# Kernel tuning notes

Measured on AMD Instinct MI355X. Metric: run time of the kernel, lower is better.

## Reference

```python
import jax, jax.numpy as jnp
import numpy as np
from jax import lax

D = 33            # n_vertices
NEG_SLOPE = 0.2   # LeakyReLU slope
EPS_IN = 1e-5     # InstanceNorm eps


def _block(x, w, b, gamma, beta):
    # Conv2d(k=3, stride=2, pad=1) -> LeakyReLU(0.2) -> optional InstanceNorm2d(affine)
    y = lax.conv_general_dilated(x, w, (2, 2), [(1, 1), (1, 1)],
                                 dimension_numbers=('NCHW', 'OIHW', 'NCHW'))
    y = y + b[None, :, None, None]
    y = jnp.where(y >= 0, y, NEG_SLOPE * y)
    if gamma is not None:
        mu = jnp.mean(y, (2, 3), keepdims=True)
        var = jnp.var(y, (2, 3), keepdims=True)
        y = (y - mu) * lax.rsqrt(var + EPS_IN) * gamma[None, :, None, None] + beta[None, :, None, None]
    return y


def _backbone(lq, w1, b1, g1, be1, w2, b2, g2, be2, w3, b3, g3, be3,
              w4, b4, g4, be4, w5, b5):
    B = lq.shape[0]
    # F.interpolate(..., 256, bilinear, align_corners=False) == half-pixel linear, no antialias
    x = jax.image.resize(lq, (B, 3, 256, 256), method='linear', antialias=False)
    x = _block(x, w1, b1, g1, be1)   # [B,16,128,128]
    x = _block(x, w2, b2, g2, be2)   # [B,32,64,64]
    x = _block(x, w3, b3, g3, be3)   # [B,64,32,32]
    x = _block(x, w4, b4, g4, be4)   # [B,128,16,16]
    x = _block(x, w5, b5, None, None)  # [B,128,8,8]; Dropout is identity in eval
    # AdaptiveAvgPool2d(2) on 8x8 -> mean over 4x4 blocks
    x = x.reshape(B, 128, 2, 4, 2, 4).mean((3, 5))  # [B,128,2,2]
    return x.reshape(B, -1)  # [B,512]


def _trilerp(lut, r, g, b):
    # lut [3,D,D,D]; r,g,b [N] in [0, D-1]; align_corners=True + border padding
    i0 = jnp.clip(jnp.floor(r).astype(jnp.int32), 0, D - 2)
    j0 = jnp.clip(jnp.floor(g).astype(jnp.int32), 0, D - 2)
    k0 = jnp.clip(jnp.floor(b).astype(jnp.int32), 0, D - 2)
    fr, fg, fb = r - i0, g - j0, b - k0

    def c(di, dj, dk):
        return lut[:, i0 + di, j0 + dj, k0 + dk]  # [3,N]

    return (c(0, 0, 0) * (1 - fr) * (1 - fg) * (1 - fb)
            + c(0, 0, 1) * (1 - fr) * (1 - fg) * fb
            + c(0, 1, 0) * (1 - fr) * fg * (1 - fb)
            + c(0, 1, 1) * (1 - fr) * fg * fb
            + c(1, 0, 0) * fr * (1 - fg) * (1 - fb)
            + c(1, 0, 1) * fr * (1 - fg) * fb
            + c(1, 1, 0) * fr * fg * (1 - fb)
            + c(1, 1, 1) * fr * fg * fb)


def _ailut_transform(img, luts, vertices):
    # img [B,3,H,W] in [0,1]; luts [B,3,D,D,D]; vertices [B,3,D] sorted in [0,1]
    B, C, H, W = img.shape
    p = img.reshape(B, C, -1)  # [B,3,N]
    # per-(b,c) searchsorted(right=True)
    idx = jax.vmap(jax.vmap(lambda v, x: jnp.searchsorted(v, x, side='right')))(vertices, p)
    idx = jnp.clip(idx, 1, D - 1)
    v_lo = jnp.take_along_axis(vertices, idx - 1, axis=-1)
    v_hi = jnp.take_along_axis(vertices, idx, axis=-1)
    frac = (p - v_lo) / (v_hi - v_lo + 1e-8)
    coord = (idx - 1).astype(img.dtype) + frac        # [B,3,N] in [0, D-1]
    coord = jnp.clip(coord, 0.0, D - 1.0)             # border padding
    # torch grid layout (blue->W, green->H, red->D); LUT axes are (red, green, blue)
    sampled = jax.vmap(_trilerp)(luts, coord[:, 0], coord[:, 1], coord[:, 2])  # [B,3,N]
    return sampled.reshape(B, C, H, W)


def _forward(lq, w1, b1, g1, be1, w2, b2, g2, be2, w3, b3, g3, be3,
             w4, b4, g4, be4, w5, b5, lw, lb, bw, aw, ab):
    B = lq.shape[0]
    codes = _backbone(lq, w1, b1, g1, be1, w2, b2, g2, be2, w3, b3, g3, be3,
                      w4, b4, g4, be4, w5, b5)          # [B,512]
    # LUTGenerator
    weights = codes @ lw.T + lb                          # [B,3]
    luts = (weights @ bw.T).reshape(B, 3, D, D, D)       # [B,3,D,D,D]
    # AdaInt
    intervals = (codes @ aw.T + ab).reshape(B, 3, D - 1)
    intervals = jax.nn.softmax(intervals, axis=-1)
    vertices = jnp.pad(jnp.cumsum(intervals, axis=-1), ((0, 0), (0, 0), (1, 0)))  # [B,3,D]
    outs = jnp.clip(_ailut_transform(lq, luts, vertices), 0.0, 1.0)
    return outs, weights, vertices


def setup_inputs() -> dict:
    key = jax.random.key(0)
    ks = jax.random.split(key, 16)
    B = 4
    lq = jax.random.uniform(ks[0], (B, 3, 1024, 1024), jnp.float32)

    def cw(k, o, i):
        return jax.random.normal(k, (o, i, 3, 3), jnp.float32) * (1.0 / np.sqrt(i * 9))

    w1 = cw(ks[1], 16, 3);   b1 = jnp.zeros(16);  g1 = jnp.ones(16);  be1 = jnp.zeros(16)
    w2 = cw(ks[2], 32, 16);  b2 = jnp.zeros(32);  g2 = jnp.ones(32);  be2 = jnp.zeros(32)
    w3 = cw(ks[3], 64, 32);  b3 = jnp.zeros(64);  g3 = jnp.ones(64);  be3 = jnp.zeros(64)
    w4 = cw(ks[4], 128, 64); b4 = jnp.zeros(128); g4 = jnp.ones(128); be4 = jnp.zeros(128)
    w5 = cw(ks[5], 128, 128); b5 = jnp.zeros(128)

    lw = jax.random.normal(ks[6], (3, 512), jnp.float32) * 0.02
    lb = jnp.ones(3, jnp.float32)  # init: bias = ones
    # basis LUT bank: rank0 = identity LUT (meshgrid/(D-1), channel-flipped), others small
    grid = jnp.stack(jnp.meshgrid(jnp.arange(D), jnp.arange(D), jnp.arange(D),
                                  indexing='ij'), 0).astype(jnp.float32) / (D - 1)
    identity = grid[::-1].reshape(-1, 1)  # [3*D^3,1]
    bw = jnp.concatenate([identity,
                          jax.random.normal(ks[7], (3 * D ** 3, 2), jnp.float32) * 0.01], axis=1)
    aw = jax.random.normal(ks[8], (96, 512), jnp.float32) * 0.01
    ab = jnp.ones(96, jnp.float32)  # init: bias = ones
    return {'lq': lq, 'w1': w1, 'b1': b1, 'g1': g1, 'be1': be1,
            'w2': w2, 'b2': b2, 'g2': g2, 'be2': be2,
            'w3': w3, 'b3': b3, 'g3': g3, 'be3': be3,
            'w4': w4, 'b4': b4, 'g4': g4, 'be4': be4,
            'w5': w5, 'b5': b5, 'lw': lw, 'lb': lb, 'bw': bw, 'aw': aw, 'ab': ab}


def reference(lq, w1, b1, g1, be1, w2, b2, g2, be2, w3, b3, g3, be3,
              w4, b4, g4, be4, w5, b5, lw, lb, bw, aw, ab):
    return _forward(lq, w1, b1, g1, be1, w2, b2, g2, be2, w3, b3, g3, be3,
                    w4, b4, g4, be4, w5, b5, lw, lb, bw, aw, ab)
```

## Files before the change

### kernel.cpp

```cpp
#include <hip/hip_runtime.h>
#include <hip/hip_fp16.h>
#include <math.h>

#define LUT_D 33
#define LUT_D3 35937
#define NEG 0.2f
#define BATCH 4
#define HW_IMG 1048576

__global__ void k_resize(const float* __restrict__ lq, float* __restrict__ out) {
    int gid = blockIdx.x * 256 + threadIdx.x;
    if (gid >= BATCH * 3 * 256 * 64) return;
    int xq = gid & 63;
    int y  = (gid >> 6) & 255;
    int pc = gid >> 14;
    const float* ra = lq + (size_t)pc * HW_IMG + (size_t)(4 * y + 1) * 1024 + xq * 16;
    const float4* pa = (const float4*)ra;
    const float4* pb = (const float4*)(ra + 1024);
    float4 a0 = pa[0], a1 = pa[1], a2 = pa[2], a3 = pa[3];
    float4 b0 = pb[0], b1 = pb[1], b2 = pb[2], b3 = pb[3];
    float4 o;
    o.x = 0.25f * (a0.y + a0.z + b0.y + b0.z);
    o.y = 0.25f * (a1.y + a1.z + b1.y + b1.z);
    o.z = 0.25f * (a2.y + a2.z + b2.y + b2.z);
    o.w = 0.25f * (a3.y + a3.z + b3.y + b3.z);
    ((float4*)out)[gid] = o;
}

template<int IC, int OC, int OH, int OW, int NSPLIT, bool NORM_IN, bool STATS_OUT>
__global__ void __launch_bounds__(256) k_conv_t(
    const float* __restrict__ in, const float* __restrict__ nrm_in,
    const float* __restrict__ w, const float* __restrict__ bias,
    float* __restrict__ out, float* __restrict__ part) {
    constexpr int IH = OH * 2, IW = OW * 2;
    constexpr int ICB = IC / NSPLIT;
    constexpr int TROW = 20, TSZ = 17 * TROW;
    constexpr int WQ = ICB * 9 / 4;
    constexpr int NTX = OW / 8, NTY = OH / 8, NOCG = OC / 16;
    constexpr int NT = NTX * NTY;
    constexpr int PX = OH * OW;

    __shared__ float sIn[ICB * TSZ];
    __shared__ float swl[16 * ICB * 9];
    __shared__ float sNm[NORM_IN ? ICB * 2 : 1];

    int id = blockIdx.x;
    int ocg   = id % NOCG;   id /= NOCG;
    int icc_i = id % NSPLIT; id /= NSPLIT;
    int tx    = id % NTX;    id /= NTX;
    int ty    = id % NTY;    id /= NTY;
    int b     = id;
    int icc   = icc_i * ICB;

    int t    = threadIdx.x;
    int lane = t >> 6;
    int px   = t & 63;
    int py   = px >> 3, pxx = px & 7;
    int oc0  = ocg * 16 + lane * 4;

    if (IC == ICB) {
        const float4* wsrc = (const float4*)(w + (size_t)ocg * 16 * IC * 9);
        for (int i = t; i < 16 * IC * 9 / 4; i += 256) ((float4*)swl)[i] = wsrc[i];
    } else {
        for (int i = t; i < 16 * WQ; i += 256) {
            int ol = i / WQ, qi = i % WQ;
            ((float4*)swl)[ol * WQ + qi] =
                *(const float4*)(w + ((size_t)(ocg * 16 + ol) * IC + icc) * 9 + qi * 4);
        }
    }
    if (NORM_IN) {
        for (int i = t; i < ICB * 2; i += 256) sNm[i] = nrm_in[(b * IC + icc) * 2 + i];
    }
    __syncthreads();

    int iy0 = ty * 16 - 1;
    int xbase = tx * 16;
    const float* inb = in + (size_t)(b * IC + icc) * (IH * IW);
    for (int q = t; q < ICB * 17 * 4; q += 256) {
        int ic_l = q / 68;
        int r    = q % 68;
        int row  = r >> 2, quad = r & 3;
        int iy = iy0 + row;
        float4 v = {0.f, 0.f, 0.f, 0.f};
        if (iy >= 0 && iy < IH) {
            v = *(const float4*)(inb + (size_t)ic_l * (IH * IW) + (size_t)iy * IW + xbase + quad * 4);
            if (NORM_IN) {
                float sc = sNm[ic_l * 2], sh = sNm[ic_l * 2 + 1];
                v.x = v.x * sc + sh; v.y = v.y * sc + sh;
                v.z = v.z * sc + sh; v.w = v.w * sc + sh;
            }
        }
        *(float4*)(sIn + ic_l * TSZ + row * TROW + 4 + quad * 4) = v;
    }
    for (int h = t; h < ICB * 17; h += 256) {
        int ic_l = h / 17, row = h % 17;
        int iy = iy0 + row, ix = xbase - 1;
        float v = 0.f;
        if (iy >= 0 && iy < IH && ix >= 0) {
            v = inb[(size_t)ic_l * (IH * IW) + (size_t)iy * IW + ix];
            if (NORM_IN) v = v * sNm[ic_l * 2] + sNm[ic_l * 2 + 1];
        }
        sIn[ic_l * TSZ + row * TROW + 3] = v;
    }
    __syncthreads();

    float acc[4];
    #pragma unroll
    for (int j = 0; j < 4; j++) acc[j] = (NSPLIT == 1) ? bias[oc0 + j] : 0.f;

    for (int i2 = 0; i2 < ICB; i2++) {
        const float* tp = sIn + i2 * TSZ + py * 2 * TROW + pxx * 2 + 3;
        float x0 = tp[0],        x1 = tp[1],        x2 = tp[2];
        float x3 = tp[TROW],     x4 = tp[TROW + 1], x5 = tp[TROW + 2];
        float x6 = tp[2 * TROW], x7 = tp[2 * TROW + 1], x8 = tp[2 * TROW + 2];
        #pragma unroll
        for (int j = 0; j < 4; j++) {
            const float* wp = swl + ((lane * 4 + j) * ICB + i2) * 9;
            acc[j] = fmaf(x0, wp[0], acc[j]);
            acc[j] = fmaf(x1, wp[1], acc[j]);
            acc[j] = fmaf(x2, wp[2], acc[j]);
            acc[j] = fmaf(x3, wp[3], acc[j]);
            acc[j] = fmaf(x4, wp[4], acc[j]);
            acc[j] = fmaf(x5, wp[5], acc[j]);
            acc[j] = fmaf(x6, wp[6], acc[j]);
            acc[j] = fmaf(x7, wp[7], acc[j]);
            acc[j] = fmaf(x8, wp[8], acc[j]);
        }
    }

    int oy = ty * 8 + py, ox = tx * 8 + pxx;
    if (NSPLIT == 1) {
        int tile = ty * NTX + tx;
        #pragma unroll
        for (int j = 0; j < 4; j++) {
            float a = acc[j];
            a = a >= 0.f ? a : NEG * a;
            out[((size_t)(b * OC + oc0 + j) * OH + oy) * OW + ox] = a;
            if (STATS_OUT) {
                float s1 = a, s2 = a * a;
                for (int off = 32; off > 0; off >>= 1) {
                    s1 += __shfl_down(s1, off, 64);
                    s2 += __shfl_down(s2, off, 64);
                }
                if (px == 0) {
                    size_t pi = ((size_t)(b * OC + oc0 + j) * NT + tile) * 2;
                    part[pi] = s1; part[pi + 1] = s2;
                }
            }
        }
    } else {
        #pragma unroll
        for (int j = 0; j < 4; j++) {
            part[(size_t)icc_i * (BATCH * OC * PX) +
                 (size_t)(b * OC + oc0 + j) * PX + oy * OW + ox] = acc[j];
        }
    }
}

template<int NSPLIT, int OC, int PX, bool STATS>
__global__ void k_combine(const float* __restrict__ ps, const float* __restrict__ bias,
                          float* __restrict__ out, float* __restrict__ spart) {
    constexpr int TOT = BATCH * OC * PX;
    int e = blockIdx.x * 256 + threadIdx.x;
    if (e >= TOT) return;
    float s = 0.f;
    #pragma unroll
    for (int k = 0; k < NSPLIT; k++) s += ps[(size_t)k * TOT + e];
    int oc = (e / PX) % OC;
    s += bias[oc];
    s = s >= 0.f ? s : NEG * s;
    out[e] = s;
    if (STATS) {
        float s1 = s, s2 = s * s;
        for (int off = 32; off > 0; off >>= 1) {
            s1 += __shfl_down(s1, off, 64);
            s2 += __shfl_down(s2, off, 64);
        }
        if ((threadIdx.x & 63) == 0) {
            int widx = e >> 6;
            spart[widx * 2] = s1; spart[widx * 2 + 1] = s2;
        }
    }
}

template<int NT>
__global__ void k_norm(const float* __restrict__ part, const float* __restrict__ g,
                       const float* __restrict__ be, float invN, int C,
                       float* __restrict__ nrm) {
    int bc = blockIdx.x;
    int t  = threadIdx.x;
    float s1 = 0.f, s2 = 0.f;
    for (int i = t; i < NT; i += 64) {
        s1 += part[((size_t)bc * NT + i) * 2];
        s2 += part[((size_t)bc * NT + i) * 2 + 1];
    }
    #pragma unroll
    for (int off = 32; off > 0; off >>= 1) {
        s1 += __shfl_down(s1, off, 64);
        s2 += __shfl_down(s2, off, 64);
    }
    if (t == 0) {
        int c = bc % C;
        float m   = s1 * invN;
        float var = s2 * invN - m * m;
        float sc  = g[c] * rsqrtf(var + 1e-5f);
        nrm[bc * 2]     = sc;
        nrm[bc * 2 + 1] = be[c] - m * sc;
    }
}

__global__ void k_pool(const float* __restrict__ f5, float* __restrict__ codes) {
    int c = blockIdx.x * 256 + threadIdx.x;
    if (c >= 2048) return;
    int b = c >> 9;
    int rest = c & 511;
    int oc = rest >> 2, q = rest & 3;
    int py = (q >> 1) * 4, px = (q & 1) * 4;
    const float* p = f5 + ((size_t)(b * 128 + oc)) * 64;
    float s = 0.f;
    #pragma unroll
    for (int dy = 0; dy < 4; dy++)
        #pragma unroll
        for (int dx = 0; dx < 4; dx++)
            s += p[(py + dy) * 8 + px + dx];
    codes[c] = s * (1.f / 16.f);
}

__global__ void k_head(const float* __restrict__ codes, const float* __restrict__ lw,
                       const float* __restrict__ lb, const float* __restrict__ aw,
                       const float* __restrict__ ab, float* __restrict__ wt,
                       float* __restrict__ vert, float* __restrict__ tabA,
                       float* __restrict__ tabC, float* __restrict__ out_w,
                       float* __restrict__ out_v) {
    int blk = blockIdx.x;
    int t = threadIdx.x;
    if (blk == 12) {
        if (t < 48) {
            int j = t >> 2, q = t & 3;
            int b = j / 3, jj = j % 3;
            const float4* c4 = (const float4*)(codes + b * 512 + q * 128);
            const float4* l4 = (const float4*)(lw + jj * 512 + q * 128);
            float s = 0.f;
            for (int k = 0; k < 32; k++) {
                float4 cv = c4[k], lv = l4[k];
                s += cv.x * lv.x + cv.y * lv.y + cv.z * lv.z + cv.w * lv.w;
            }
            s += __shfl_down(s, 2, 64);
            s += __shfl_down(s, 1, 64);
            if (q == 0) {
                s += lb[jj];
                wt[j] = s;
                out_w[j] = s;
            }
        }
        return;
    }
    int b = blk / 3, ch = blk % 3;
    __shared__ float y[32];
    __shared__ float vsh[33];
    {
        int m = t & 31, half = t >> 5;
        const float4* c4 = (const float4*)(codes + b * 512 + half * 256);
        const float4* a4 = (const float4*)(aw + (size_t)(ch * 32 + m) * 512 + half * 256);
        float s = (half == 0) ? ab[ch * 32 + m] : 0.f;
        for (int k = 0; k < 64; k++) {
            float4 cv = c4[k], av = a4[k];
            s += cv.x * av.x + cv.y * av.y + cv.z * av.z + cv.w * av.w;
        }
        s += __shfl_down(s, 32, 64);
        if (half == 0) y[m] = s;
    }
    __syncthreads();
    if (t == 0) {
        float mx = y[0];
        for (int m = 1; m < 32; m++) mx = fmaxf(mx, y[m]);
        float e[32];
        float sum = 0.f;
        for (int m = 0; m < 32; m++) { e[m] = expf(y[m] - mx); sum += e[m]; }
        float inv = 1.f / sum;
        float cum = 0.f;
        float* vb = vert + (b * 3 + ch) * 33;
        float* ob = out_v + (b * 3 + ch) * 33;
        vb[0] = 0.f; ob[0] = 0.f; vsh[0] = 0.f;
        for (int m = 0; m < 32; m++) {
            cum += e[m] * inv;
            vb[m + 1] = cum; ob[m + 1] = cum; vsh[m + 1] = cum;
        }
    }
    __syncthreads();
    float4* A4 = ((float4*)tabA) + (b * 3 + ch) * 256;
    float*  C1 = tabC + (b * 3 + ch) * 256;
    for (int u = t; u < 256; u += 64) {
        float lo = (float)u * (1.f / 256.f);
        float hi = (float)(u + 1) * (1.f / 256.f);
        int n0 = 0, nin = 0;
        float vs = 2.0f;
        #pragma unroll
        for (int m = 0; m < 33; m++) {
            float vm = vsh[m];
            n0 += (vm <= lo) ? 1 : 0;
            if (vm > lo && vm < hi) { if (nin == 0) vs = vm; nin++; }
        }
        int i0 = n0 < 1 ? 1 : (n0 > 32 ? 32 : n0);
        int i1 = (n0 + 1) < 1 ? 1 : ((n0 + 1) > 32 ? 32 : (n0 + 1));
        float m0 = 1.f / (vsh[i0] - vsh[i0 - 1] + 1e-8f);
        float c0 = (float)(i0 - 1) - vsh[i0 - 1] * m0;
        float m1 = 1.f / (vsh[i1] - vsh[i1 - 1] + 1e-8f);
        float c1 = (float)(i1 - 1) - vsh[i1 - 1] * m1;
        if (nin >= 2) { vs = 2.0f; m0 = __int_as_float(0x7fc00000); c0 = 0.f; }
        A4[u] = make_float4(vs, m0, c0, m1);
        C1[u] = c1;
    }
}

__global__ void k_lutgen(const float* __restrict__ bw, const float* __restrict__ wt,
                         float4* __restrict__ lutp) {
    int gid = blockIdx.x * 256 + threadIdx.x;
    if (gid >= BATCH * LUT_D3) return;
    int b = gid / LUT_D3;
    int cell = gid - b * LUT_D3;
    int k = cell % LUT_D;
    int cn = (k < LUT_D - 1) ? cell + 1 : cell;
    float w0 = wt[b * 3], w1 = wt[b * 3 + 1], w2 = wt[b * 3 + 2];
    const float* r0p = bw + (size_t)(0 * LUT_D3 + cell) * 3;
    const float* g0p = bw + (size_t)(1 * LUT_D3 + cell) * 3;
    const float* b0p = bw + (size_t)(2 * LUT_D3 + cell) * 3;
    const float* r1p = bw + (size_t)(0 * LUT_D3 + cn) * 3;
    const float* g1p = bw + (size_t)(1 * LUT_D3 + cn) * 3;
    const float* b1p = bw + (size_t)(2 * LUT_D3 + cn) * 3;
    union { float4 f4; __half h[8]; } u;
    u.h[0] = __float2half_rn(r0p[0] * w0 + r0p[1] * w1 + r0p[2] * w2);
    u.h[1] = __float2half_rn(g0p[0] * w0 + g0p[1] * w1 + g0p[2] * w2);
    u.h[2] = __float2half_rn(b0p[0] * w0 + b0p[1] * w1 + b0p[2] * w2);
    u.h[3] = __float2half_rn(r1p[0] * w0 + r1p[1] * w1 + r1p[2] * w2);
    u.h[4] = __float2half_rn(g1p[0] * w0 + g1p[1] * w1 + g1p[2] * w2);
    u.h[5] = __float2half_rn(b1p[0] * w0 + b1p[1] * w1 + b1p[2] * w2);
    u.h[6] = __float2half_rn(0.f);
    u.h[7] = __float2half_rn(0.f);
    lutp[gid] = u.f4;
}

__global__ void k_cellgen(const float4* __restrict__ lutp, float4* __restrict__ cells) {
    int gid = blockIdx.x * 256 + threadIdx.x;
    if (gid >= BATCH * 32768) return;
    int b = gid >> 15;
    int cell = gid & 32767;
    int k0 = cell & 31, j0 = (cell >> 5) & 31, i0 = cell >> 10;
    const float4* L = lutp + (size_t)b * LUT_D3;
    int base = (i0 * LUT_D + j0) * LUT_D + k0;
    float4 e00 = L[base];
    float4 e01 = L[base + LUT_D];
    float4 e10 = L[base + LUT_D * LUT_D];
    float4 e11 = L[base + LUT_D * LUT_D + LUT_D];
    float4 o0, o1, o2;
    o0.x = e00.x; o0.y = e00.y; o0.z = e00.z;
    o0.w = e01.x; o1.x = e01.y; o1.y = e01.z;
    o1.z = e10.x; o1.w = e10.y; o2.x = e10.z;
    o2.y = e11.x; o2.z = e11.y; o2.w = e11.z;
    float4* dst = cells + (size_t)gid * 4;
    dst[0] = o0; dst[1] = o1; dst[2] = o2;
}

__device__ __forceinline__ void searchL(const float4* __restrict__ A,
                                        const float* __restrict__ C,
                                        const float* __restrict__ v33,
                                        float x, int& i0, float& f) {
    int u = (int)(x * 256.f);
    u = u < 0 ? 0 : (u > 255 ? 255 : u);
    float4 e = A[u];
    float c1 = C[u];
    float coord = (x < e.x) ? fmaf(e.y, x, e.z) : fmaf(e.w, x, c1);
    if (!(coord == coord)) {
        int lo = 0, hi = LUT_D;
        while (lo < hi) { int mid = (lo + hi) >> 1; if (v33[mid] <= x) lo = mid + 1; else hi = mid; }
        int idx = lo < 1 ? 1 : (lo > LUT_D - 1 ? LUT_D - 1 : lo);
        float vl = v33[idx - 1], vh = v33[idx];
        coord = (float)(idx - 1) + (x - vl) / (vh - vl + 1e-8f);
    }
    coord = fminf(fmaxf(coord, 0.f), (float)(LUT_D - 1));
    i0 = (int)coord;
    if (i0 > LUT_D - 2) i0 = LUT_D - 2;
    f = coord - (float)i0;
}

__device__ __forceinline__ void decode_lerp3(float wa, float wb, float wc, float fb,
                                             float& rv, float& gv, float& bv) {
    union { float f; __half2 h; } u0, u1, u2;
    u0.f = wa; u1.f = wb; u2.f = wc;
    float2 a = __half22float2(u0.h);
    float2 b = __half22float2(u1.h);
    float2 c = __half22float2(u2.h);
    rv = fmaf(fb, b.y - a.x, a.x);
    gv = fmaf(fb, c.x - a.y, a.y);
    bv = fmaf(fb, c.y - b.x, b.x);
}

__global__ void __launch_bounds__(256) k_transform(const float* __restrict__ lq,
                                                   const float4* __restrict__ cells,
                                                   const float* __restrict__ vert,
                                                   const float* __restrict__ gA,
                                                   const float* __restrict__ gC,
                                                   float* __restrict__ out) {
    int bimg = blockIdx.x >> 10;
    int blk  = blockIdx.x & 1023;
    __shared__ float4 sA[3 * 256];
    __shared__ float  sC[3 * 256];
    __shared__ float  sv[3 * LUT_D + 1];

    int p0 = blk * 1024 + threadIdx.x * 4;
    const float* lr = lq + (size_t)bimg * 3 * HW_IMG + p0;
    float4 r4 = *(const float4*)(lr);
    float4 g4 = *(const float4*)(lr + HW_IMG);
    float4 b4 = *(const float4*)(lr + 2 * HW_IMG);

    const float4* gA4 = (const float4*)gA;
    for (int i = threadIdx.x; i < 768; i += 256) sA[i] = gA4[bimg * 768 + i];
    for (int i = threadIdx.x; i < 192; i += 256)
        ((float4*)sC)[i] = ((const float4*)gC)[bimg * 192 + i];
    if (threadIdx.x < 99) sv[threadIdx.x] = vert[bimg * 99 + threadIdx.x];
    __syncthreads();

    float rr[4] = {r4.x, r4.y, r4.z, r4.w};
    float gg[4] = {g4.x, g4.y, g4.z, g4.w};
    float bb[4] = {b4.x, b4.y, b4.z, b4.w};

    int cidx[4];
    float fra[4], fga[4], fba[4];
    #pragma unroll
    for (int i = 0; i < 4; i++) {
        int i0, j0, k0;
        searchL(sA,       sC,       sv,      rr[i], i0, fra[i]);
        searchL(sA + 256, sC + 256, sv + 33, gg[i], j0, fga[i]);
        searchL(sA + 512, sC + 512, sv + 66, bb[i], k0, fba[i]);
        cidx[i] = ((i0 * 32 + j0) << 5) + k0;
    }
    float4 c0[4], c1[4], c2[4];
    #pragma unroll
    for (int i = 0; i < 4; i++) {
        const float4* p = cells + (((size_t)(bimg << 15) + cidx[i]) << 2);
        c0[i] = p[0]; c1[i] = p[1]; c2[i] = p[2];
    }
    float ro[4], go[4], bo[4];
    #pragma unroll
    for (int i = 0; i < 4; i++) {
        float fb = fba[i];
        float r00, g00, b00, r01, g01, b01, r10, g10, b10, r11, g11, b11;
        decode_lerp3(c0[i].x, c0[i].y, c0[i].z, fb, r00, g00, b00);
        decode_lerp3(c0[i].w, c1[i].x, c1[i].y, fb, r01, g01, b01);
        decode_lerp3(c1[i].z, c1[i].w, c2[i].x, fb, r10, g10, b10);
        decode_lerp3(c2[i].y, c2[i].z, c2[i].w, fb, r11, g11, b11);
        float fr = fra[i], fg = fga[i];
        float w00 = (1.f - fr) * (1.f - fg), w01 = (1.f - fr) * fg;
        float w10 = fr * (1.f - fg),         w11 = fr * fg;
        float rx = r00 * w00 + r01 * w01 + r10 * w10 + r11 * w11;
        float ry = g00 * w00 + g01 * w01 + g10 * w10 + g11 * w11;
        float rz = b00 * w00 + b01 * w01 + b10 * w10 + b11 * w11;
        ro[i] = fminf(fmaxf(rx, 0.f), 1.f);
        go[i] = fminf(fmaxf(ry, 0.f), 1.f);
        bo[i] = fminf(fmaxf(rz, 0.f), 1.f);
    }
    float* op = out + (size_t)bimg * 3 * HW_IMG + p0;
    float4 o0 = {ro[0], ro[1], ro[2], ro[3]};
    float4 o1 = {go[0], go[1], go[2], go[3]};
    float4 o2 = {bo[0], bo[1], bo[2], bo[3]};
    *(float4*)(op) = o0;
    *(float4*)(op + HW_IMG) = o1;
    *(float4*)(op + 2 * HW_IMG) = o2;
}

extern "C" void kernel_launch(void* const* d_in, const int* in_sizes, int n_in,
                              void* d_out, int out_size, void* d_ws, size_t ws_size,
                              hipStream_t stream) {
    const float* lq  = (const float*)d_in[0];
    const float* w1  = (const float*)d_in[1];
    const float* b1  = (const float*)d_in[2];
    const float* g1  = (const float*)d_in[3];
    const float* be1 = (const float*)d_in[4];
    const float* w2  = (const float*)d_in[5];
    const float* b2  = (const float*)d_in[6];
    const float* g2  = (const float*)d_in[7];
    const float* be2 = (const float*)d_in[8];
    const float* w3  = (const float*)d_in[9];
    const float* b3  = (const float*)d_in[10];
    const float* g3  = (const float*)d_in[11];
    const float* be3 = (const float*)d_in[12];
    const float* w4  = (const float*)d_in[13];
    const float* b4  = (const float*)d_in[14];
    const float* g4  = (const float*)d_in[15];
    const float* be4 = (const float*)d_in[16];
    const float* w5  = (const float*)d_in[17];
    const float* b5  = (const float*)d_in[18];
    const float* lw  = (const float*)d_in[19];
    const float* lb  = (const float*)d_in[20];
    const float* bw  = (const float*)d_in[21];
    const float* aw  = (const float*)d_in[22];
    const float* ab  = (const float*)d_in[23];

    float* ws     = (float*)d_ws;
    float* r256   = ws;
    float* f1     = r256 + 786432;
    float* f2     = f1 + 1048576;
    float* f3     = f2 + 524288;
    float* f4     = f3 + 262144;
    float* f5     = f4 + 131072;
    float* codes  = f5 + 32768;
    float* wt     = codes + 2048;
    float* vert   = wt + 12;
    float* part1  = vert + 396;
    float* part2  = part1 + 32768;
    float* part3  = part2 + 16384;
    float* spart4 = part3 + 8192;
    float* norm1  = spart4 + 4096;
    float* norm2  = norm1 + 128;
    float* norm3  = norm2 + 256;
    float* norm4  = norm3 + 512;
    float* tabA   = norm4 + 1024;
    float* tabC   = tabA + 12288;
    float* luts4  = tabC + 3072;
    float* psplit4 = f1;
    float* psplit5 = f1 + 524288;
    float* cells  = ws;

    float* outs  = (float*)d_out;
    float* out_w = outs + (size_t)BATCH * 3 * HW_IMG;
    float* out_v = out_w + 12;

    k_resize<<<768, 256, 0, stream>>>(lq, r256);
    k_conv_t<3, 16, 128, 128, 1, false, true><<<1024, 256, 0, stream>>>(
        r256, nullptr, w1, b1, f1, part1);
    k_norm<256><<<64, 64, 0, stream>>>(part1, g1, be1, 1.f / 16384.f, 16, norm1);
    k_conv_t<16, 32, 64, 64, 1, true, true><<<512, 256, 0, stream>>>(
        f1, norm1, w2, b2, f2, part2);
    k_norm<64><<<128, 64, 0, stream>>>(part2, g2, be2, 1.f / 4096.f, 32, norm2);
    k_conv_t<32, 64, 32, 32, 1, true, true><<<256, 256, 0, stream>>>(
        f2, norm2, w3, b3, f3, part3);
    k_norm<16><<<256, 64, 0, stream>>>(part3, g3, be3, 1.f / 1024.f, 64, norm3);
    k_conv_t<64, 128, 16, 16, 4, true, false><<<512, 256, 0, stream>>>(
        f3, norm3, w4, b4, nullptr, psplit4);
    k_combine<4, 128, 256, true><<<512, 256, 0, stream>>>(psplit4, b4, f4, spart4);
    k_norm<4><<<512, 64, 0, stream>>>(spart4, g4, be4, 1.f / 256.f, 128, norm4);
    k_conv_t<128, 128, 8, 8, 8, true, false><<<256, 256, 0, stream>>>(
        f4, norm4, w5, b5, nullptr, psplit5);
    k_combine<8, 128, 64, false><<<128, 256, 0, stream>>>(psplit5, b5, f5, nullptr);
    k_pool<<<8, 256, 0, stream>>>(f5, codes);
    k_head<<<13, 64, 0, stream>>>(codes, lw, lb, aw, ab, wt, vert, tabA, tabC, out_w, out_v);
    k_lutgen<<<(BATCH * LUT_D3 + 255) / 256, 256, 0, stream>>>(bw, wt, (float4*)luts4);
    k_cellgen<<<512, 256, 0, stream>>>((const float4*)luts4, (float4*)cells);
    k_transform<<<BATCH * 1024, 256, 0, stream>>>(
        lq, (const float4*)cells, vert, tabA, tabC, outs);
}
```

Before: 284.3 us.

## Fuse resize, norm, split-combine, pool and LUT generation into fewer kernels

Folds the resize into the first conv's tile load, computes the instance-norm scale and shift inside each consumer conv from the partial sums, and replaces the input-channel split plus combine kernels with in-block channel chunking. Pooling moves into the head kernel, LUT generation and cell packing merge into one kernel that emits half-precision cells, and the search tables are repacked into a single five-float layout. The transform kernel also remaps block indices by XCD. Launch count drops from 17 to 8, but the late conv layers now run with only 128 and 32 blocks, which leaves much of the GPU idle, and fp16 cells lose LUT precision.

Measured after the change: 326.8 us. +15.0%, slower.

```diff
diff --git a/kernel.cpp b/kernel.cpp
--- a/kernel.cpp
+++ b/kernel.cpp
@@ -8,49 +8,27 @@
 #define BATCH 4
 #define HW_IMG 1048576
 
-__global__ void k_resize(const float* __restrict__ lq, float* __restrict__ out) {
-    int gid = blockIdx.x * 256 + threadIdx.x;
-    if (gid >= BATCH * 3 * 256 * 64) return;
-    int xq = gid & 63;
-    int y  = (gid >> 6) & 255;
-    int pc = gid >> 14;
-    const float* ra = lq + (size_t)pc * HW_IMG + (size_t)(4 * y + 1) * 1024 + xq * 16;
-    const float4* pa = (const float4*)ra;
-    const float4* pb = (const float4*)(ra + 1024);
-    float4 a0 = pa[0], a1 = pa[1], a2 = pa[2], a3 = pa[3];
-    float4 b0 = pb[0], b1 = pb[1], b2 = pb[2], b3 = pb[3];
-    float4 o;
-    o.x = 0.25f * (a0.y + a0.z + b0.y + b0.z);
-    o.y = 0.25f * (a1.y + a1.z + b1.y + b1.z);
-    o.z = 0.25f * (a2.y + a2.z + b2.y + b2.z);
-    o.w = 0.25f * (a3.y + a3.z + b3.y + b3.z);
-    ((float4*)out)[gid] = o;
-}
-
-template<int IC, int OC, int OH, int OW, int NSPLIT, bool NORM_IN, bool STATS_OUT>
-__global__ void __launch_bounds__(256) k_conv_t(
-    const float* __restrict__ in, const float* __restrict__ nrm_in,
+template<int IC, int OC, int OH, int OW, int ICCH, bool NORM_IN, bool RESIZE_IN, bool STATS_OUT>
+__global__ void __launch_bounds__(256) k_conv2(
+    const float* __restrict__ in, const float* __restrict__ part_in,
+    const float* __restrict__ g, const float* __restrict__ be, float invN, int ntin,
     const float* __restrict__ w, const float* __restrict__ bias,
-    float* __restrict__ out, float* __restrict__ part) {
+    float* __restrict__ out, float* __restrict__ part_out) {
     constexpr int IH = OH * 2, IW = OW * 2;
-    constexpr int ICB = IC / NSPLIT;
+    constexpr int NCH = IC / ICCH;
     constexpr int TROW = 20, TSZ = 17 * TROW;
-    constexpr int WQ = ICB * 9 / 4;
     constexpr int NTX = OW / 8, NTY = OH / 8, NOCG = OC / 16;
     constexpr int NT = NTX * NTY;
-    constexpr int PX = OH * OW;
-
-    __shared__ float sIn[ICB * TSZ];
-    __shared__ float swl[16 * ICB * 9];
-    __shared__ float sNm[NORM_IN ? ICB * 2 : 1];
+
+    __shared__ float sIn[ICCH * TSZ];
+    __shared__ float swl[16 * ICCH * 9];
+    __shared__ float sNm[NORM_IN ? IC * 2 : 1];
 
     int id = blockIdx.x;
-    int ocg   = id % NOCG;   id /= NOCG;
-    int icc_i = id % NSPLIT; id /= NSPLIT;
-    int tx    = id % NTX;    id /= NTX;
-    int ty    = id % NTY;    id /= NTY;
-    int b     = id;
-    int icc   = icc_i * ICB;
+    int ocg = id % NOCG;  id /= NOCG;
+    int tx  = id % NTX;   id /= NTX;
+    int ty  = id % NTY;   id /= NTY;
+    int b   = id;
 
     int t    = threadIdx.x;
     int lane = t >> 6;
@@ -58,187 +36,187 @@
     int py   = px >> 3, pxx = px & 7;
     int oc0  = ocg * 16 + lane * 4;
 
-    if (IC == ICB) {
-        const float4* wsrc = (const float4*)(w + (size_t)ocg * 16 * IC * 9);
-        for (int i = t; i < 16 * IC * 9 / 4; i += 256) ((float4*)swl)[i] = wsrc[i];
-    } else {
-        for (int i = t; i < 16 * WQ; i += 256) {
-            int ol = i / WQ, qi = i % WQ;
-            ((float4*)swl)[ol * WQ + qi] =
-                *(const float4*)(w + ((size_t)(ocg * 16 + ol) * IC + icc) * 9 + qi * 4);
-        }
-    }
     if (NORM_IN) {
-        for (int i = t; i < ICB * 2; i += 256) sNm[i] = nrm_in[(b * IC + icc) * 2 + i];
-    }
-    __syncthreads();
+        constexpr int P = 256 / IC;
+        int c = t / P, r = t % P;
+        float s1 = 0.f, s2 = 0.f;
+        for (int i = r; i < ntin; i += P) {
+            const float* pp = part_in + ((size_t)(b * IC + c) * ntin + i) * 2;
+            s1 += pp[0]; s2 += pp[1];
+        }
+        #pragma unroll
+        for (int off = P >> 1; off > 0; off >>= 1) {
+            s1 += __shfl_down(s1, off, 64);
+            s2 += __shfl_down(s2, off, 64);
+        }
+        if (r == 0) {
+            float m   = s1 * invN;
+            float var = s2 * invN - m * m;
+            float sc  = g[c] * rsqrtf(var + 1e-5f);
+            sNm[c * 2]     = sc;
+            sNm[c * 2 + 1] = be[c] - m * sc;
+        }
+        __syncthreads();
+    }
+
+    float acc[4];
+    #pragma unroll
+    for (int j = 0; j < 4; j++) acc[j] = bias[oc0 + j];
 
     int iy0 = ty * 16 - 1;
     int xbase = tx * 16;
-    const float* inb = in + (size_t)(b * IC + icc) * (IH * IW);
-    for (int q = t; q < ICB * 17 * 4; q += 256) {
-        int ic_l = q / 68;
-        int r    = q % 68;
-        int row  = r >> 2, quad = r & 3;
-        int iy = iy0 + row;
-        float4 v = {0.f, 0.f, 0.f, 0.f};
-        if (iy >= 0 && iy < IH) {
-            v = *(const float4*)(inb + (size_t)ic_l * (IH * IW) + (size_t)iy * IW + xbase + quad * 4);
-            if (NORM_IN) {
-                float sc = sNm[ic_l * 2], sh = sNm[ic_l * 2 + 1];
-                v.x = v.x * sc + sh; v.y = v.y * sc + sh;
-                v.z = v.z * sc + sh; v.w = v.w * sc + sh;
-            }
-        }
-        *(float4*)(sIn + ic_l * TSZ + row * TROW + 4 + quad * 4) = v;
-    }
-    for (int h = t; h < ICB * 17; h += 256) {
-        int ic_l = h / 17, row = h % 17;
-        int iy = iy0 + row, ix = xbase - 1;
-        float v = 0.f;
-        if (iy >= 0 && iy < IH && ix >= 0) {
-            v = inb[(size_t)ic_l * (IH * IW) + (size_t)iy * IW + ix];
-            if (NORM_IN) v = v * sNm[ic_l * 2] + sNm[ic_l * 2 + 1];
-        }
-        sIn[ic_l * TSZ + row * TROW + 3] = v;
-    }
-    __syncthreads();
-
-    float acc[4];
-    #pragma unroll
-    for (int j = 0; j < 4; j++) acc[j] = (NSPLIT == 1) ? bias[oc0 + j] : 0.f;
-
-    for (int i2 = 0; i2 < ICB; i2++) {
-        const float* tp = sIn + i2 * TSZ + py * 2 * TROW + pxx * 2 + 3;
-        float x0 = tp[0],        x1 = tp[1],        x2 = tp[2];
-        float x3 = tp[TROW],     x4 = tp[TROW + 1], x5 = tp[TROW + 2];
-        float x6 = tp[2 * TROW], x7 = tp[2 * TROW + 1], x8 = tp[2 * TROW + 2];
-        #pragma unroll
-        for (int j = 0; j < 4; j++) {
-            const float* wp = swl + ((lane * 4 + j) * ICB + i2) * 9;
-            acc[j] = fmaf(x0, wp[0], acc[j]);
-            acc[j] = fmaf(x1, wp[1], acc[j]);
-            acc[j] = fmaf(x2, wp[2], acc[j]);
-            acc[j] = fmaf(x3, wp[3], acc[j]);
-            acc[j] = fmaf(x4, wp[4], acc[j]);
-            acc[j] = fmaf(x5, wp[5], acc[j]);
-            acc[j] = fmaf(x6, wp[6], acc[j]);
-            acc[j] = fmaf(x7, wp[7], acc[j]);
-            acc[j] = fmaf(x8, wp[8], acc[j]);
+
+    for (int ch = 0; ch < NCH; ch++) {
+        int icc = ch * ICCH;
+        if (ch) __syncthreads();
+
+        if (IC == ICCH) {
+            const float4* wsrc = (const float4*)(w + (size_t)ocg * 16 * IC * 9);
+            for (int i = t; i < 16 * IC * 9 / 4; i += 256) ((float4*)swl)[i] = wsrc[i];
+        } else {
+            constexpr int WQ = ICCH * 9 / 4;
+            for (int i = t; i < 16 * WQ; i += 256) {
+                int ol = i / WQ, qi = i % WQ;
+                ((float4*)swl)[ol * WQ + qi] =
+                    *(const float4*)(w + ((size_t)(ocg * 16 + ol) * IC + icc) * 9 + qi * 4);
+            }
+        }
+
+        if (RESIZE_IN) {
+            for (int q = t; q < ICCH * 17 * 4; q += 256) {
+                int ic_l = q / 68;
+                int r2   = q % 68;
+                int row  = r2 >> 2, quad = r2 & 3;
+                int iy = iy0 + row;
+                float4 v = {0.f, 0.f, 0.f, 0.f};
+                if (iy >= 0 && iy < IH) {
+                    const float* lb_ = in + (size_t)(b * IC + icc + ic_l) * HW_IMG
+                                          + (size_t)(4 * iy + 1) * 1024;
+                    int c0 = (xbase + quad * 4) * 4;
+                    const float4* pa = (const float4*)(lb_ + c0);
+                    const float4* pb = (const float4*)(lb_ + 1024 + c0);
+                    float4 a0 = pa[0], a1 = pa[1], a2 = pa[2], a3 = pa[3];
+                    float4 q0 = pb[0], q1 = pb[1], q2 = pb[2], q3 = pb[3];
+                    v.x = 0.25f * (a0.y + a0.z + q0.y + q0.z);
+                    v.y = 0.25f * (a1.y + a1.z + q1.y + q1.z);
+                    v.z = 0.25f * (a2.y + a2.z + q2.y + q2.z);
+                    v.w = 0.25f * (a3.y + a3.z + q3.y + q3.z);
+                }
+                *(float4*)(sIn + ic_l * TSZ + row * TROW + 4 + quad * 4) = v;
+            }
+            for (int h = t; h < ICCH * 17; h += 256) {
+                int ic_l = h / 17, row = h % 17;
+                int iy = iy0 + row, ix = xbase - 1;
+                float v = 0.f;
+                if (iy >= 0 && iy < IH && ix >= 0) {
+                    const float* lb_ = in + (size_t)(b * IC + icc + ic_l) * HW_IMG
+                                          + (size_t)(4 * iy + 1) * 1024;
+                    float4 a = *(const float4*)(lb_ + ix * 4);
+                    float4 q0 = *(const float4*)(lb_ + 1024 + ix * 4);
+                    v = 0.25f * (a.y + a.z + q0.y + q0.z);
+                }
+                sIn[ic_l * TSZ + row * TROW + 3] = v;
+            }
+        } else {
+            const float* inb = in + (size_t)(b * IC + icc) * (IH * IW);
+            for (int q = t; q < ICCH * 17 * 4; q += 256) {
+                int ic_l = q / 68;
+                int r2   = q % 68;
+                int row  = r2 >> 2, quad = r2 & 3;
+                int iy = iy0 + row;
+                float4 v = {0.f, 0.f, 0.f, 0.f};
+                if (iy >= 0 && iy < IH) {
+                    v = *(const float4*)(inb + (size_t)ic_l * (IH * IW)
+                                             + (size_t)iy * IW + xbase + quad * 4);
+                    if (NORM_IN) {
+                        float sc = sNm[(icc + ic_l) * 2], sh = sNm[(icc + ic_l) * 2 + 1];
+                        v.x = v.x * sc + sh; v.y = v.y * sc + sh;
+                        v.z = v.z * sc + sh; v.w = v.w * sc + sh;
+                    }
+                }
+                *(float4*)(sIn + ic_l * TSZ + row * TROW + 4 + quad * 4) = v;
+            }
+            for (int h = t; h < ICCH * 17; h += 256) {
+                int ic_l = h / 17, row = h % 17;
+                int iy = iy0 + row, ix = xbase - 1;
+                float v = 0.f;
+                if (iy >= 0 && iy < IH && ix >= 0) {
+                    v = inb[(size_t)ic_l * (IH * IW) + (size_t)iy * IW + ix];
+                    if (NORM_IN) v = v * sNm[(icc + ic_l) * 2] + sNm[(icc + ic_l) * 2 + 1];
+                }
+                sIn[ic_l * TSZ + row * TROW + 3] = v;
+            }
+        }
+        __syncthreads();
+
+        for (int i2 = 0; i2 < ICCH; i2++) {
+            const float* tp = sIn + i2 * TSZ + py * 2 * TROW + pxx * 2 + 3;
+            float x0 = tp[0],        x1 = tp[1],        x2 = tp[2];
+            float x3 = tp[TROW],     x4 = tp[TROW + 1], x5 = tp[TROW + 2];
+            float x6 = tp[2 * TROW], x7 = tp[2 * TROW + 1], x8 = tp[2 * TROW + 2];
+            #pragma unroll
+            for (int j = 0; j < 4; j++) {
+                const float* wp = swl + ((lane * 4 + j) * ICCH + i2) * 9;
+                acc[j] = fmaf(x0, wp[0], acc[j]);
+                acc[j] = fmaf(x1, wp[1], acc[j]);
+                acc[j] = fmaf(x2, wp[2], acc[j]);
+                acc[j] = fmaf(x3, wp[3], acc[j]);
+                acc[j] = fmaf(x4, wp[4], acc[j]);
+                acc[j] = fmaf(x5, wp[5], acc[j]);
+                acc[j] = fmaf(x6, wp[6], acc[j]);
+                acc[j] = fmaf(x7, wp[7], acc[j]);
+                acc[j] = fmaf(x8, wp[8], acc[j]);
+            }
         }
     }
 
     int oy = ty * 8 + py, ox = tx * 8 + pxx;
-    if (NSPLIT == 1) {
-        int tile = ty * NTX + tx;
-        #pragma unroll
-        for (int j = 0; j < 4; j++) {
-            float a = acc[j];
-            a = a >= 0.f ? a : NEG * a;
-            out[((size_t)(b * OC + oc0 + j) * OH + oy) * OW + ox] = a;
-            if (STATS_OUT) {
-                float s1 = a, s2 = a * a;
-                for (int off = 32; off > 0; off >>= 1) {
-                    s1 += __shfl_down(s1, off, 64);
-                    s2 += __shfl_down(s2, off, 64);
-                }
-                if (px == 0) {
-                    size_t pi = ((size_t)(b * OC + oc0 + j) * NT + tile) * 2;
-                    part[pi] = s1; part[pi + 1] = s2;
-                }
-            }
-        }
-    } else {
-        #pragma unroll
-        for (int j = 0; j < 4; j++) {
-            part[(size_t)icc_i * (BATCH * OC * PX) +
-                 (size_t)(b * OC + oc0 + j) * PX + oy * OW + ox] = acc[j];
-        }
-    }
-}
-
-template<int NSPLIT, int OC, int PX, bool STATS>
-__global__ void k_combine(const float* __restrict__ ps, const float* __restrict__ bias,
-                          float* __restrict__ out, float* __restrict__ spart) {
-    constexpr int TOT = BATCH * OC * PX;
-    int e = blockIdx.x * 256 + threadIdx.x;
-    if (e >= TOT) return;
-    float s = 0.f;
-    #pragma unroll
-    for (int k = 0; k < NSPLIT; k++) s += ps[(size_t)k * TOT + e];
-    int oc = (e / PX) % OC;
-    s += bias[oc];
-    s = s >= 0.f ? s : NEG * s;
-    out[e] = s;
-    if (STATS) {
-        float s1 = s, s2 = s * s;
-        for (int off = 32; off > 0; off >>= 1) {
-            s1 += __shfl_down(s1, off, 64);
-            s2 += __shfl_down(s2, off, 64);
-        }
-        if ((threadIdx.x & 63) == 0) {
-            int widx = e >> 6;
-            spart[widx * 2] = s1; spart[widx * 2 + 1] = s2;
-        }
-    }
-}
-
-template<int NT>
-__global__ void k_norm(const float* __restrict__ part, const float* __restrict__ g,
-                       const float* __restrict__ be, float invN, int C,
-                       float* __restrict__ nrm) {
-    int bc = blockIdx.x;
-    int t  = threadIdx.x;
-    float s1 = 0.f, s2 = 0.f;
-    for (int i = t; i < NT; i += 64) {
-        s1 += part[((size_t)bc * NT + i) * 2];
-        s2 += part[((size_t)bc * NT + i) * 2 + 1];
-    }
-    #pragma unroll
-    for (int off = 32; off > 0; off >>= 1) {
-        s1 += __shfl_down(s1, off, 64);
-        s2 += __shfl_down(s2, off, 64);
-    }
-    if (t == 0) {
-        int c = bc % C;
-        float m   = s1 * invN;
-        float var = s2 * invN - m * m;
-        float sc  = g[c] * rsqrtf(var + 1e-5f);
-        nrm[bc * 2]     = sc;
-        nrm[bc * 2 + 1] = be[c] - m * sc;
-    }
-}
-
-__global__ void k_pool(const float* __restrict__ f5, float* __restrict__ codes) {
-    int c = blockIdx.x * 256 + threadIdx.x;
-    if (c >= 2048) return;
-    int b = c >> 9;
-    int rest = c & 511;
-    int oc = rest >> 2, q = rest & 3;
-    int py = (q >> 1) * 4, px = (q & 1) * 4;
-    const float* p = f5 + ((size_t)(b * 128 + oc)) * 64;
-    float s = 0.f;
-    #pragma unroll
-    for (int dy = 0; dy < 4; dy++)
-        #pragma unroll
-        for (int dx = 0; dx < 4; dx++)
-            s += p[(py + dy) * 8 + px + dx];
-    codes[c] = s * (1.f / 16.f);
-}
-
-__global__ void k_head(const float* __restrict__ codes, const float* __restrict__ lw,
+    int tile = ty * NTX + tx;
+    #pragma unroll
+    for (int j = 0; j < 4; j++) {
+        float a = acc[j];
+        a = a >= 0.f ? a : NEG * a;
+        out[((size_t)(b * OC + oc0 + j) * OH + oy) * OW + ox] = a;
+        if (STATS_OUT) {
+            float s1 = a, s2 = a * a;
+            for (int off = 32; off > 0; off >>= 1) {
+                s1 += __shfl_down(s1, off, 64);
+                s2 += __shfl_down(s2, off, 64);
+            }
+            if (px == 0) {
+                size_t pi = ((size_t)(b * OC + oc0 + j) * NT + tile) * 2;
+                part_out[pi] = s1; part_out[pi + 1] = s2;
+            }
+        }
+    }
+}
+
+__global__ void k_head(const float* __restrict__ f5, const float* __restrict__ lw,
                        const float* __restrict__ lb, const float* __restrict__ aw,
                        const float* __restrict__ ab, float* __restrict__ wt,
-                       float* __restrict__ vert, float* __restrict__ tabA,
-                       float* __restrict__ tabC, float* __restrict__ out_w,
-                       float* __restrict__ out_v) {
+                       float* __restrict__ vert, float* __restrict__ gT,
+                       float* __restrict__ out_w, float* __restrict__ out_v) {
     int blk = blockIdx.x;
     int t = threadIdx.x;
     if (blk == 12) {
+        __shared__ float sc2[2048];
+        for (int s = t; s < 2048; s += 64) {
+            int b = s >> 9, rest = s & 511, oc = rest >> 2, q = rest & 3;
+            int py = (q >> 1) * 4, pxq = (q & 1) * 4;
+            const float* p = f5 + (size_t)(b * 128 + oc) * 64;
+            float sum = 0.f;
+            #pragma unroll
+            for (int dy = 0; dy < 4; dy++) {
+                float4 v = *(const float4*)(p + (py + dy) * 8 + pxq);
+                sum += v.x + v.y + v.z + v.w;
+            }
+            sc2[s] = sum * (1.f / 16.f);
+        }
+        __syncthreads();
         if (t < 48) {
             int j = t >> 2, q = t & 3;
             int b = j / 3, jj = j % 3;
-            const float4* c4 = (const float4*)(codes + b * 512 + q * 128);
+            const float4* c4 = (const float4*)(sc2 + b * 512 + q * 128);
             const float4* l4 = (const float4*)(lw + jj * 512 + q * 128);
             float s = 0.f;
             for (int k = 0; k < 32; k++) {
@@ -247,20 +225,30 @@
             }
             s += __shfl_down(s, 2, 64);
             s += __shfl_down(s, 1, 64);
-            if (q == 0) {
-                s += lb[jj];
-                wt[j] = s;
-                out_w[j] = s;
-            }
+            if (q == 0) { s += lb[jj]; wt[j] = s; out_w[j] = s; }
         }
         return;
     }
     int b = blk / 3, ch = blk % 3;
+    __shared__ float scode[512];
     __shared__ float y[32];
     __shared__ float vsh[33];
+    for (int s = t; s < 512; s += 64) {
+        int oc = s >> 2, q = s & 3;
+        int py = (q >> 1) * 4, pxq = (q & 1) * 4;
+        const float* p = f5 + (size_t)(b * 128 + oc) * 64;
+        float sum = 0.f;
+        #pragma unroll
+        for (int dy = 0; dy < 4; dy++) {
+            float4 v = *(const float4*)(p + (py + dy) * 8 + pxq);
+            sum += v.x + v.y + v.z + v.w;
+        }
+        scode[s] = sum * (1.f / 16.f);
+    }
+    __syncthreads();
     {
         int m = t & 31, half = t >> 5;
-        const float4* c4 = (const float4*)(codes + b * 512 + half * 256);
+        const float4* c4 = (const float4*)(scode + half * 256);
         const float4* a4 = (const float4*)(aw + (size_t)(ch * 32 + m) * 512 + half * 256);
         float s = (half == 0) ? ab[ch * 32 + m] : 0.f;
         for (int k = 0; k < 64; k++) {
@@ -288,8 +276,7 @@
         }
     }
     __syncthreads();
-    float4* A4 = ((float4*)tabA) + (b * 3 + ch) * 256;
-    float*  C1 = tabC + (b * 3 + ch) * 256;
+    float* T = gT + (size_t)(b * 3 + ch) * 1280;
     for (int u = t; u < 256; u += 64) {
         float lo = (float)u * (1.f / 256.f);
         float hi = (float)(u + 1) * (1.f / 256.f);
@@ -308,68 +295,54 @@
         float m1 = 1.f / (vsh[i1] - vsh[i1 - 1] + 1e-8f);
         float c1 = (float)(i1 - 1) - vsh[i1 - 1] * m1;
         if (nin >= 2) { vs = 2.0f; m0 = __int_as_float(0x7fc00000); c0 = 0.f; }
-        A4[u] = make_float4(vs, m0, c0, m1);
-        C1[u] = c1;
-    }
-}
-
-__global__ void k_lutgen(const float* __restrict__ bw, const float* __restrict__ wt,
-                         float4* __restrict__ lutp) {
-    int gid = blockIdx.x * 256 + threadIdx.x;
-    if (gid >= BATCH * LUT_D3) return;
-    int b = gid / LUT_D3;
-    int cell = gid - b * LUT_D3;
-    int k = cell % LUT_D;
-    int cn = (k < LUT_D - 1) ? cell + 1 : cell;
-    float w0 = wt[b * 3], w1 = wt[b * 3 + 1], w2 = wt[b * 3 + 2];
-    const float* r0p = bw + (size_t)(0 * LUT_D3 + cell) * 3;
-    const float* g0p = bw + (size_t)(1 * LUT_D3 + cell) * 3;
-    const float* b0p = bw + (size_t)(2 * LUT_D3 + cell) * 3;
-    const float* r1p = bw + (size_t)(0 * LUT_D3 + cn) * 3;
-    const float* g1p = bw + (size_t)(1 * LUT_D3 + cn) * 3;
-    const float* b1p = bw + (size_t)(2 * LUT_D3 + cn) * 3;
-    union { float4 f4; __half h[8]; } u;
-    u.h[0] = __float2half_rn(r0p[0] * w0 + r0p[1] * w1 + r0p[2] * w2);
-    u.h[1] = __float2half_rn(g0p[0] * w0 + g0p[1] * w1 + g0p[2] * w2);
-    u.h[2] = __float2half_rn(b0p[0] * w0 + b0p[1] * w1 + b0p[2] * w2);
-    u.h[3] = __float2half_rn(r1p[0] * w0 + r1p[1] * w1 + r1p[2] * w2);
-    u.h[4] = __float2half_rn(g1p[0] * w0 + g1p[1] * w1 + g1p[2] * w2);
-    u.h[5] = __float2half_rn(b1p[0] * w0 + b1p[1] * w1 + b1p[2] * w2);
-    u.h[6] = __float2half_rn(0.f);
-    u.h[7] = __float2half_rn(0.f);
-    lutp[gid] = u.f4;
-}
-
-__global__ void k_cellgen(const float4* __restrict__ lutp, float4* __restrict__ cells) {
+        T[u * 5]     = vs;
+        T[u * 5 + 1] = m0;
+        T[u * 5 + 2] = c0;
+        T[u * 5 + 3] = m1;
+        T[u * 5 + 4] = c1;
+    }
+}
+
+__global__ void k_cells(const float* __restrict__ bw, const float* __restrict__ wtp,
+                        float4* __restrict__ cells) {
     int gid = blockIdx.x * 256 + threadIdx.x;
     if (gid >= BATCH * 32768) return;
     int b = gid >> 15;
     int cell = gid & 32767;
     int k0 = cell & 31, j0 = (cell >> 5) & 31, i0 = cell >> 10;
-    const float4* L = lutp + (size_t)b * LUT_D3;
-    int base = (i0 * LUT_D + j0) * LUT_D + k0;
-    float4 e00 = L[base];
-    float4 e01 = L[base + LUT_D];
-    float4 e10 = L[base + LUT_D * LUT_D];
-    float4 e11 = L[base + LUT_D * LUT_D + LUT_D];
-    float4 o0, o1, o2;
-    o0.x = e00.x; o0.y = e00.y; o0.z = e00.z;
-    o0.w = e01.x; o1.x = e01.y; o1.y = e01.z;
-    o1.z = e10.x; o1.w = e10.y; o2.x = e10.z;
-    o2.y = e11.x; o2.z = e11.y; o2.w = e11.z;
+    float w0 = wtp[b * 3], w1 = wtp[b * 3 + 1], w2 = wtp[b * 3 + 2];
+    int ci[4] = { (i0 * 33 + j0) * 33 + k0,
+                  (i0 * 33 + j0 + 1) * 33 + k0,
+                  ((i0 + 1) * 33 + j0) * 33 + k0,
+                  ((i0 + 1) * 33 + j0 + 1) * 33 + k0 };
+    float h[24];
+    #pragma unroll
+    for (int c = 0; c < 4; c++) {
+        #pragma unroll
+        for (int kk = 0; kk < 2; kk++) {
+            int id2 = ci[c] + kk;
+            #pragma unroll
+            for (int pl = 0; pl < 3; pl++) {
+                const float* p = bw + ((size_t)(pl * LUT_D3 + id2)) * 3;
+                h[c * 6 + kk * 3 + pl] = p[0] * w0 + p[1] * w1 + p[2] * w2;
+            }
+        }
+    }
+    union { float4 f4[3]; __half hh[24]; } u;
+    #pragma unroll
+    for (int i = 0; i < 24; i++) u.hh[i] = __float2half_rn(h[i]);
     float4* dst = cells + (size_t)gid * 4;
-    dst[0] = o0; dst[1] = o1; dst[2] = o2;
-}
-
-__device__ __forceinline__ void searchL(const float4* __restrict__ A,
-                                        const float* __restrict__ C,
-                                        const float* __restrict__ v33,
-                                        float x, int& i0, float& f) {
+    dst[0] = u.f4[0]; dst[1] = u.f4[1]; dst[2] = u.f4[2];
+}
+
+__device__ __forceinline__ void searchL5(const float* __restrict__ T,
+                                         const float* __restrict__ v33,
+                                         float x, int& i0, float& f) {
     int u = (int)(x * 256.f);
     u = u < 0 ? 0 : (u > 255 ? 255 : u);
-    float4 e = A[u];
-    float c1 = C[u];
-    float coord = (x < e.x) ? fmaf(e.y, x, e.z) : fmaf(e.w, x, c1);
+    const float* e = T + u * 5;
+    float vs = e[0];
+    float coord = (x < vs) ? fmaf(e[1], x, e[2]) : fmaf(e[3], x, e[4]);
     if (!(coord == coord)) {
         int lo = 0, hi = LUT_D;
         while (lo < hi) { int mid = (lo + hi) >> 1; if (v33[mid] <= x) lo = mid + 1; else hi = mid; }
@@ -398,14 +371,15 @@
 __global__ void __launch_bounds__(256) k_transform(const float* __restrict__ lq,
                                                    const float4* __restrict__ cells,
                                                    const float* __restrict__ vert,
-                                                   const float* __restrict__ gA,
-                                                   const float* __restrict__ gC,
+                                                   const float* __restrict__ gT,
                                                    float* __restrict__ out) {
-    int bimg = blockIdx.x >> 10;
-    int blk  = blockIdx.x & 1023;
-    __shared__ float4 sA[3 * 256];
-    __shared__ float  sC[3 * 256];
-    __shared__ float  sv[3 * LUT_D + 1];
+    int orig = blockIdx.x;
+    int xcd  = orig & 7;
+    int bimg = xcd >> 1;
+    int blk  = ((orig >> 3) << 1) | (xcd & 1);
+
+    __shared__ float sT[3840];
+    __shared__ float sv[100];
 
     int p0 = blk * 1024 + threadIdx.x * 4;
     const float* lr = lq + (size_t)bimg * 3 * HW_IMG + p0;
@@ -413,10 +387,7 @@
     float4 g4 = *(const float4*)(lr + HW_IMG);
     float4 b4 = *(const float4*)(lr + 2 * HW_IMG);
 
-    const float4* gA4 = (const float4*)gA;
-    for (int i = threadIdx.x; i < 768; i += 256) sA[i] = gA4[bimg * 768 + i];
-    for (int i = threadIdx.x; i < 192; i += 256)
-        ((float4*)sC)[i] = ((const float4*)gC)[bimg * 192 + i];
+    for (int i = threadIdx.x; i < 3840; i += 256) sT[i] = gT[bimg * 3840 + i];
     if (threadIdx.x < 99) sv[threadIdx.x] = vert[bimg * 99 + threadIdx.x];
     __syncthreads();
 
@@ -429,9 +400,9 @@
     #pragma unroll
     for (int i = 0; i < 4; i++) {
         int i0, j0, k0;
-        searchL(sA,       sC,       sv,      rr[i], i0, fra[i]);
-        searchL(sA + 256, sC + 256, sv + 33, gg[i], j0, fga[i]);
-        searchL(sA + 512, sC + 512, sv + 66, bb[i], k0, fba[i]);
+        searchL5(sT,        sv,      rr[i], i0, fra[i]);
+        searchL5(sT + 1280, sv + 33, gg[i], j0, fga[i]);
+        searchL5(sT + 2560, sv + 66, bb[i], k0, fba[i]);
         cidx[i] = ((i0 * 32 + j0) << 5) + k0;
     }
     float4 c0[4], c1[4], c2[4];
@@ -496,56 +467,37 @@
     const float* aw  = (const float*)d_in[22];
     const float* ab  = (const float*)d_in[23];
 
-    float* ws     = (float*)d_ws;
-    float* r256   = ws;
-    float* f1     = r256 + 786432;
-    float* f2     = f1 + 1048576;
-    float* f3     = f2 + 524288;
-    float* f4     = f3 + 262144;
-    float* f5     = f4 + 131072;
-    float* codes  = f5 + 32768;
-    float* wt     = codes + 2048;
-    float* vert   = wt + 12;
-    float* part1  = vert + 396;
-    float* part2  = part1 + 32768;
-    float* part3  = part2 + 16384;
-    float* spart4 = part3 + 8192;
-    float* norm1  = spart4 + 4096;
-    float* norm2  = norm1 + 128;
-    float* norm3  = norm2 + 256;
-    float* norm4  = norm3 + 512;
-    float* tabA   = norm4 + 1024;
-    float* tabC   = tabA + 12288;
-    float* luts4  = tabC + 3072;
-    float* psplit4 = f1;
-    float* psplit5 = f1 + 524288;
-    float* cells  = ws;
+    float* ws    = (float*)d_ws;
+    float* cells = ws;
+    float* f1    = ws;
+    float* f2    = f1 + 1048576;
+    float* f3    = f2 + 524288;
+    float* f4    = f3 + 262144;
+    float* f5    = f4 + 131072;
+    float* tail  = ws + 2097152;
+    float* wt    = tail;
+    float* vert  = wt + 12;
+    float* part1 = vert + 396;
+    float* part2 = part1 + 32768;
+    float* part3 = part2 + 16384;
+    float* part4 = part3 + 8192;
+    float* gT    = part4 + 4096;
 
     float* outs  = (float*)d_out;
     float* out_w = outs + (size_t)BATCH * 3 * HW_IMG;
     float* out_v = out_w + 12;
 
-    k_resize<<<768, 256, 0, stream>>>(lq, r256);
-    k_conv_t<3, 16, 128, 128, 1, false, true><<<1024, 256, 0, stream>>>(
-        r256, nullptr, w1, b1, f1, part1);
-    k_norm<256><<<64, 64, 0, stream>>>(part1, g1, be1, 1.f / 16384.f, 16, norm1);
-    k_conv_t<16, 32, 64, 64, 1, true, true><<<512, 256, 0, stream>>>(
-        f1, norm1, w2, b2, f2, part2);
-    k_norm<64><<<128, 64, 0, stream>>>(part2, g2, be2, 1.f / 4096.f, 32, norm2);
-    k_conv_t<32, 64, 32, 32, 1, true, true><<<256, 256, 0, stream>>>(
-        f2, norm2, w3, b3, f3, part3);
-    k_norm<16><<<256, 64, 0, stream>>>(part3, g3, be3, 1.f / 1024.f, 64, norm3);
-    k_conv_t<64, 128, 16, 16, 4, true, false><<<512, 256, 0, stream>>>(
-        f3, norm3, w4, b4, nullptr, psplit4);
-    k_combine<4, 128, 256, true><<<512, 256, 0, stream>>>(psplit4, b4, f4, spart4);
-    k_norm<4><<<512, 64, 0, stream>>>(spart4, g4, be4, 1.f / 256.f, 128, norm4);
-    k_conv_t<128, 128, 8, 8, 8, true, false><<<256, 256, 0, stream>>>(
-        f4, norm4, w5, b5, nullptr, psplit5);
-    k_combine<8, 128, 64, false><<<128, 256, 0, stream>>>(psplit5, b5, f5, nullptr);
-    k_pool<<<8, 256, 0, stream>>>(f5, codes);
-    k_head<<<13, 64, 0, stream>>>(codes, lw, lb, aw, ab, wt, vert, tabA, tabC, out_w, out_v);
-    k_lutgen<<<(BATCH * LUT_D3 + 255) / 256, 256, 0, stream>>>(bw, wt, (float4*)luts4);
-    k_cellgen<<<512, 256, 0, stream>>>((const float4*)luts4, (float4*)cells);
-    k_transform<<<BATCH * 1024, 256, 0, stream>>>(
-        lq, (const float4*)cells, vert, tabA, tabC, outs);
-}
+    k_conv2<3, 16, 128, 128, 3, false, true, true><<<1024, 256, 0, stream>>>(
+        lq, nullptr, nullptr, nullptr, 0.f, 0, w1, b1, f1, part1);
+    k_conv2<16, 32, 64, 64, 16, true, false, true><<<512, 256, 0, stream>>>(
+        f1, part1, g1, be1, 1.f / 16384.f, 256, w2, b2, f2, part2);
+    k_conv2<32, 64, 32, 32, 32, true, false, true><<<256, 256, 0, stream>>>(
+        f2, part2, g2, be2, 1.f / 4096.f, 64, w3, b3, f3, part3);
+    k_conv2<64, 128, 16, 16, 32, true, false, true><<<128, 256, 0, stream>>>(
+        f3, part3, g3, be3, 1.f / 1024.f, 16, w4, b4, f4, part4);
+    k_conv2<128, 128, 8, 8, 32, true, false, false><<<32, 256, 0, stream>>>(
+        f4, part4, g4, be4, 1.f / 256.f, 4, w5, b5, f5, nullptr);
+    k_head<<<13, 64, 0, stream>>>(f5, lw, lb, aw, ab, wt, vert, gT, out_w, out_v);
+    k_cells<<<512, 256, 0, stream>>>(bw, wt, (float4*)cells);
+    k_transform<<<BATCH * 1024, 256, 0, stream>>>(lq, (const float4*)cells, vert, gT, outs);
+}
```
